# Kernel optimization log

Hardware: AMD Instinct MI355X
Metric: run time of the kernel (lower is better)

## Reference

```python
import jax, jax.numpy as jnp
import numpy as np

SIZE = 512
N_STROKES = 8
N_SAMPLES = 32
STROKE_WIDTH = 0.04


def setup_inputs() -> dict:
    key = jax.random.key(0)
    k1, _ = jax.random.split(key)
    # control points seeded like torch.rand(...) * 0.6 + 0.2
    control_points = jax.random.uniform(k1, (N_STROKES, 4, 2), dtype=jnp.float32) * 0.6 + 0.2
    # pixel grid buffer: (x, y) coords in [0,1], row-major over (y, x)
    coords = jnp.linspace(0.0, 1.0, SIZE, dtype=jnp.float32)
    grid_y, grid_x = jnp.meshgrid(coords, coords, indexing="ij")
    pixel_grid = jnp.stack([grid_x, grid_y], axis=-1).reshape(-1, 2)  # (HW, 2)
    return {"control_points": control_points, "pixel_grid": pixel_grid}


def _bezier3_samples(curves, n_samples):
    # curves: (S, 4, 2) -> (S, n_samples, 2)
    ts = jnp.linspace(0.0, 1.0, n_samples, dtype=curves.dtype)
    t = ts[None, :, None]
    mt = 1.0 - t
    p0, p1, p2, p3 = (curves[:, k:k + 1, :] for k in range(4))
    return mt ** 3 * p0 + 3.0 * mt ** 2 * t * p1 + 3.0 * mt * t ** 2 * p2 + t ** 3 * p3


def reference(control_points, pixel_grid):
    # all_strokes(): symmetric=False, empty stroke_groups -> just clamp
    pts = jnp.clip(control_points, 0.0, 1.0)
    samples = _bezier3_samples(pts, N_SAMPLES).reshape(-1, 2)  # (P, 2), P = S*n_samples
    sharpness = float(N_SAMPLES) * 8.0
    # pairwise distances (HW, P) — soft-min via logsumexp over curve points
    diff = pixel_grid[:, None, :] - samples[None, :, :]          # (HW, P, 2)
    dist = jnp.sqrt(jnp.sum(diff * diff, axis=-1))               # (HW, P)
    min_dist = -jax.nn.logsumexp(-sharpness * dist, axis=-1) / sharpness  # (HW,)
    coverage = jax.nn.sigmoid((STROKE_WIDTH - min_dist) * (8.0 / STROKE_WIDTH))
    return (1.0 - coverage.reshape(SIZE, SIZE))[None]  # (1, H, W)
```

## Files before the change

kernel.cpp:

```cpp
#include <hip/hip_runtime.h>


#define SIZE 512
#define RADIUS 0.06f
#define FARCUT 0.1217f
#define HB 0.00684932f
#define HD 0.00968631f

__device__ __forceinline__ float clamp01(float x) {
    return fminf(fmaxf(x, 0.0f), 1.0f);
}
__device__ __forceinline__ float wave_min(float v) {
    #pragma unroll
    for (int m = 1; m < 64; m <<= 1) v = fminf(v, __shfl_xor(v, m));
    return v;
}

__global__ __launch_bounds__(64) void bezier_glyph_kernel(
        const float* __restrict__ cp,
        float* __restrict__ out)
{
    __shared__ float2 list[260];

    const int tid = threadIdx.x;
    const int b   = blockIdx.x;
    const int row_base = (b >> 6) << 3;
    const int col_base = (b & 63) << 3;
    const float inv = 1.0f / 511.0f;
    const float cx  = ((float)col_base + 3.5f) * inv;
    const float cy  = ((float)row_base + 3.5f) * inv;

    float sxv[4], syv[4], bb2v[4];
    {
        const int s = tid >> 3;
        const float* p = cp + s * 8;
        const float x0 = clamp01(p[0]), y0 = clamp01(p[1]);
        const float x1 = clamp01(p[2]), y1 = clamp01(p[3]);
        const float x2 = clamp01(p[4]), y2 = clamp01(p[5]);
        const float x3 = clamp01(p[6]), y3 = clamp01(p[7]);
        const float c1x = 3.0f * (x1 - x0);
        const float c2x = 3.0f * (x0 - 2.0f * x1 + x2);
        const float c3x = x3 - x0 + 3.0f * (x1 - x2);
        const float c1y = 3.0f * (y1 - y0);
        const float c2y = 3.0f * (y0 - 2.0f * y1 + y2);
        const float c3y = y3 - y0 + 3.0f * (y1 - y2);
        #pragma unroll
        for (int r = 0; r < 4; ++r) {
            const int j    = ((tid << 2) + r) & 31;
            const float u  = (float)j * (1.0f / 31.0f);
            const float sx = fmaf(fmaf(fmaf(c3x, u, c2x), u, c1x), u, x0);
            const float sy = fmaf(fmaf(fmaf(c3y, u, c2y), u, c1y), u, y0);
            sxv[r] = sx; syv[r] = sy;
            const float bx = fmaxf(fabsf(sx - cx) - HB, 0.0f);
            const float by = fmaxf(fabsf(sy - cy) - HB, 0.0f);
            bb2v[r] = fmaf(bx, bx, by * by);
        }
    }

    const float A = __builtin_amdgcn_sqrtf(wave_min(
        fminf(fminf(bb2v[0], bb2v[1]), fminf(bb2v[2], bb2v[3]))));

    const int row = row_base + (tid >> 3);
    const int col = col_base + (tid & 7);

    if (A > FARCUT) {
        out[row * SIZE + col] = 1.0f;
        return;
    }

    const float T   = fminf(A + 2.0f * HD, FARCUT) + RADIUS + 1e-4f;
    const float Ts  = T * T;
    const unsigned long long lt = (1ull << tid) - 1ull;
    int n = 0;
    #pragma unroll
    for (int r = 0; r < 4; ++r) {
        const bool keep = (bb2v[r] <= Ts);
        const unsigned long long mk = __ballot(keep);
        if (keep)
            list[n + (int)__popcll(mk & lt)] = make_float2(sxv[r], syv[r]);
        n += (int)__popcll(mk);
    }
    if (tid < 4) list[n + tid] = make_float2(1e3f, 1e3f);
    __syncthreads();

    const float py = (float)row * inv;
    const float px = (float)col * inv;
    const float C  = 369.3299304675766f;
    const float nC = -C;
    const float cA = C * A;
    float S = 0.0f;
    const int nr = (n + 3) & ~3;
    for (int k = 0; k < nr; k += 4) {
        const float2 a = list[k],     b2 = list[k + 1];
        const float2 c = list[k + 2], e  = list[k + 3];
        float dx, dy;
        dx = px - a.x;  dy = py - a.y;  const float qa = fmaf(dx, dx, dy * dy);
        dx = px - b2.x; dy = py - b2.y; const float qb = fmaf(dx, dx, dy * dy);
        dx = px - c.x;  dy = py - c.y;  const float qc = fmaf(dx, dx, dy * dy);
        dx = px - e.x;  dy = py - e.y;  const float qe = fmaf(dx, dx, dy * dy);
        S += __builtin_amdgcn_exp2f(fmaf(nC, __builtin_amdgcn_sqrtf(qa), cA))
           + __builtin_amdgcn_exp2f(fmaf(nC, __builtin_amdgcn_sqrtf(qb), cA))
           + __builtin_amdgcn_exp2f(fmaf(nC, __builtin_amdgcn_sqrtf(qc), cA))
           + __builtin_amdgcn_exp2f(fmaf(nC, __builtin_amdgcn_sqrtf(qe), cA));
    }

    const float md = A - __builtin_amdgcn_logf(S) * (1.0f / C);
    const float K  = 288.53900817779268f;
    out[row * SIZE + col] = __builtin_amdgcn_rcpf(
        1.0f + __builtin_amdgcn_exp2f((0.04f - md) * K));
}

extern "C" void kernel_launch(void* const* d_in, const int* in_sizes, int n_in,
                              void* d_out, int out_size, void* d_ws, size_t ws_size,
                              hipStream_t stream) {
    const float* cp = (const float*)d_in[0];
    float* out = (float*)d_out;
    bezier_glyph_kernel<<<dim3(4096), dim3(64), 0, stream>>>(cp, out);
}
```

Before: 58.81 us.

## Split per-tile sample loop across four waves with shared-memory partial sums

Blocks grow from one wave to four. Each thread now evaluates one curve sample, and the per-wave minimum and keep-counts are combined through shared memory. Each wave then handles a strided quarter of the filtered sample list for the same 8x8 pixel tile, and wave 0 reduces the four partial sums before writing the output. The aim is to shorten the serial exp/sqrt loop per tile and raise parallelism, at the cost of extra barriers, redundant threads in far tiles, and fewer resident blocks per CU.

Result: no change. 59.10 us (+0.5%).

```diff
diff --git a/kernel.cpp b/kernel.cpp
--- a/kernel.cpp
+++ b/kernel.cpp
@@ -16,23 +16,28 @@
     return v;
 }
 
-__global__ __launch_bounds__(64) void bezier_glyph_kernel(
+__global__ __launch_bounds__(256) void bezier_glyph_kernel(
         const float* __restrict__ cp,
         float* __restrict__ out)
 {
-    __shared__ float2 list[260];
+    __shared__ float2 list[264];
+    __shared__ float  wred[4];
+    __shared__ int    cnt[4];
+    __shared__ float  part[4][64];
 
-    const int tid = threadIdx.x;
-    const int b   = blockIdx.x;
+    const int tid  = threadIdx.x;
+    const int w    = tid >> 6;
+    const int lane = tid & 63;
+    const int b    = blockIdx.x;
     const int row_base = (b >> 6) << 3;
     const int col_base = (b & 63) << 3;
     const float inv = 1.0f / 511.0f;
     const float cx  = ((float)col_base + 3.5f) * inv;
     const float cy  = ((float)row_base + 3.5f) * inv;
 
-    float sxv[4], syv[4], bb2v[4];
+    float sx, sy, bb2;
     {
-        const int s = tid >> 3;
+        const int s = tid >> 5;
         const float* p = cp + s * 8;
         const float x0 = clamp01(p[0]), y0 = clamp01(p[1]);
         const float x1 = clamp01(p[2]), y1 = clamp01(p[3]);
@@ -44,42 +49,42 @@
         const float c1y = 3.0f * (y1 - y0);
         const float c2y = 3.0f * (y0 - 2.0f * y1 + y2);
         const float c3y = y3 - y0 + 3.0f * (y1 - y2);
-        #pragma unroll
-        for (int r = 0; r < 4; ++r) {
-            const int j    = ((tid << 2) + r) & 31;
-            const float u  = (float)j * (1.0f / 31.0f);
-            const float sx = fmaf(fmaf(fmaf(c3x, u, c2x), u, c1x), u, x0);
-            const float sy = fmaf(fmaf(fmaf(c3y, u, c2y), u, c1y), u, y0);
-            sxv[r] = sx; syv[r] = sy;
-            const float bx = fmaxf(fabsf(sx - cx) - HB, 0.0f);
-            const float by = fmaxf(fabsf(sy - cy) - HB, 0.0f);
-            bb2v[r] = fmaf(bx, bx, by * by);
-        }
+        const float u   = (float)(tid & 31) * (1.0f / 31.0f);
+        sx = fmaf(fmaf(fmaf(c3x, u, c2x), u, c1x), u, x0);
+        sy = fmaf(fmaf(fmaf(c3y, u, c2y), u, c1y), u, y0);
+        const float bx = fmaxf(fabsf(sx - cx) - HB, 0.0f);
+        const float by = fmaxf(fabsf(sy - cy) - HB, 0.0f);
+        bb2 = fmaf(bx, bx, by * by);
     }
 
-    const float A = __builtin_amdgcn_sqrtf(wave_min(
-        fminf(fminf(bb2v[0], bb2v[1]), fminf(bb2v[2], bb2v[3]))));
+    const float wm = wave_min(bb2);
+    if (lane == 0) wred[w] = wm;
+    __syncthreads();
+    const float A = __builtin_amdgcn_sqrtf(
+        fminf(fminf(wred[0], wred[1]), fminf(wred[2], wred[3])));
 
-    const int row = row_base + (tid >> 3);
-    const int col = col_base + (tid & 7);
+    const int row = row_base + (lane >> 3);
+    const int col = col_base + (lane & 7);
 
     if (A > FARCUT) {
-        out[row * SIZE + col] = 1.0f;
+        if (w == 0) out[row * SIZE + col] = 1.0f;
         return;
     }
 
     const float T   = fminf(A + 2.0f * HD, FARCUT) + RADIUS + 1e-4f;
     const float Ts  = T * T;
-    const unsigned long long lt = (1ull << tid) - 1ull;
-    int n = 0;
-    #pragma unroll
-    for (int r = 0; r < 4; ++r) {
-        const bool keep = (bb2v[r] <= Ts);
-        const unsigned long long mk = __ballot(keep);
-        if (keep)
-            list[n + (int)__popcll(mk & lt)] = make_float2(sxv[r], syv[r]);
-        n += (int)__popcll(mk);
-    }
+    const bool  keep = (bb2 <= Ts);
+    const unsigned long long mk = __ballot(keep);
+    const unsigned long long lt = (1ull << lane) - 1ull;
+    if (lane == 0) cnt[w] = (int)__popcll(mk);
+    __syncthreads();
+    const int c0 = cnt[0], c1 = cnt[1], c2 = cnt[2], c3 = cnt[3];
+    const int n  = c0 + c1 + c2 + c3;
+    int off = 0;
+    if (w > 0) off += c0;
+    if (w > 1) off += c1;
+    if (w > 2) off += c2;
+    if (keep) list[off + (int)__popcll(mk & lt)] = make_float2(sx, sy);
     if (tid < 4) list[n + tid] = make_float2(1e3f, 1e3f);
     __syncthreads();
 
@@ -88,9 +93,9 @@
     const float C  = 369.3299304675766f;
     const float nC = -C;
     const float cA = C * A;
-    float S = 0.0f;
+    float S0 = 0.0f, S1 = 0.0f, S2 = 0.0f, S3 = 0.0f;
     const int nr = (n + 3) & ~3;
-    for (int k = 0; k < nr; k += 4) {
+    for (int k = (w << 2); k < nr; k += 16) {
         const float2 a = list[k],     b2 = list[k + 1];
         const float2 c = list[k + 2], e  = list[k + 3];
         float dx, dy;
@@ -98,16 +103,22 @@
         dx = px - b2.x; dy = py - b2.y; const float qb = fmaf(dx, dx, dy * dy);
         dx = px - c.x;  dy = py - c.y;  const float qc = fmaf(dx, dx, dy * dy);
         dx = px - e.x;  dy = py - e.y;  const float qe = fmaf(dx, dx, dy * dy);
-        S += __builtin_amdgcn_exp2f(fmaf(nC, __builtin_amdgcn_sqrtf(qa), cA))
-           + __builtin_amdgcn_exp2f(fmaf(nC, __builtin_amdgcn_sqrtf(qb), cA))
-           + __builtin_amdgcn_exp2f(fmaf(nC, __builtin_amdgcn_sqrtf(qc), cA))
-           + __builtin_amdgcn_exp2f(fmaf(nC, __builtin_amdgcn_sqrtf(qe), cA));
+        S0 += __builtin_amdgcn_exp2f(fmaf(nC, __builtin_amdgcn_sqrtf(qa), cA));
+        S1 += __builtin_amdgcn_exp2f(fmaf(nC, __builtin_amdgcn_sqrtf(qb), cA));
+        S2 += __builtin_amdgcn_exp2f(fmaf(nC, __builtin_amdgcn_sqrtf(qc), cA));
+        S3 += __builtin_amdgcn_exp2f(fmaf(nC, __builtin_amdgcn_sqrtf(qe), cA));
     }
+    part[w][lane] = (S0 + S1) + (S2 + S3);
+    __syncthreads();
 
-    const float md = A - __builtin_amdgcn_logf(S) * (1.0f / C);
-    const float K  = 288.53900817779268f;
-    out[row * SIZE + col] = __builtin_amdgcn_rcpf(
-        1.0f + __builtin_amdgcn_exp2f((0.04f - md) * K));
+    if (w == 0) {
+        const float S = (part[0][lane] + part[1][lane])
+                      + (part[2][lane] + part[3][lane]);
+        const float md = A - __builtin_amdgcn_logf(S) * (1.0f / C);
+        const float K  = 288.53900817779268f;
+        out[row * SIZE + col] = __builtin_amdgcn_rcpf(
+            1.0f + __builtin_amdgcn_exp2f((0.04f - md) * K));
+    }
 }
 
 extern "C" void kernel_launch(void* const* d_in, const int* in_sizes, int n_in,
@@ -115,5 +126,5 @@
                               hipStream_t stream) {
     const float* cp = (const float*)d_in[0];
     float* out = (float*)d_out;
-    bezier_glyph_kernel<<<dim3(4096), dim3(64), 0, stream>>>(cp, out);
+    bezier_glyph_kernel<<<dim3(4096), dim3(256), 0, stream>>>(cp, out);
 }
```
